# Optimization experiments

Measured on AMD Instinct MI355X. Metric: run time of the kernel, lower is better.

## Reference

```python
import jax, jax.numpy as jnp
import numpy as np

NUM_HEADS = 1
HIDDEN = 256
HEAD_DIM = HIDDEN // NUM_HEADS
SCALE = HEAD_DIM ** -0.5


def _rotate_pairwise(x):
    # (... , d) -> rotate adjacent pairs: (x0,x1,x2,x3,..) -> (-x1,x0,-x3,x2,..)
    shape = x.shape
    x = x.reshape(*shape[:-1], -1, 2)
    x = jnp.stack([-x[..., 1], x[..., 0]], axis=-1)
    return x.reshape(shape)


def setup_inputs() -> dict:
    key = jax.random.key(0)
    ks = jax.random.split(key, 12)
    B, PB, QS, KS = 1, 1, 4096, 16448
    KV_IN = 64
    d = {
        'query': jax.random.normal(ks[0], (B, PB, QS, HIDDEN), jnp.float32),
        'key': jax.random.normal(ks[1], (B, PB, KS, KV_IN), jnp.float32),
        'value': jax.random.normal(ks[2], (B, PB, KS, KV_IN), jnp.float32),
        'rope_cos': jax.random.normal(ks[3], (QS, HEAD_DIM), jnp.float32),
        'rope_sin': jax.random.normal(ks[4], (QS, HEAD_DIM), jnp.float32),
        'wq': jax.random.normal(ks[5], (HIDDEN, HIDDEN), jnp.float32) * (HIDDEN ** -0.5),
        'bq': jnp.zeros((HIDDEN,), jnp.float32),
        'wk': jax.random.normal(ks[6], (KV_IN, HIDDEN), jnp.float32) * (KV_IN ** -0.5),
        'bk': jnp.zeros((HIDDEN,), jnp.float32),
        'wv': jax.random.normal(ks[7], (KV_IN, HIDDEN), jnp.float32) * (KV_IN ** -0.5),
        'bv': jnp.zeros((HIDDEN,), jnp.float32),
        'wo': jax.random.normal(ks[8], (HIDDEN, HIDDEN), jnp.float32) * (HIDDEN ** -0.5),
        'bo': jnp.zeros((HIDDEN,), jnp.float32),
        'num_k_exclude_rope': 64,
    }
    return d


def reference(query, key, value, rope_cos, rope_sin, wq, bq, wk, bk, wv, bv, wo, bo, num_k_exclude_rope):
    batch, pb, qs, _ = query.shape
    ks = key.shape[2]
    B = batch * pb
    # projections -> [B, H, S, hd]
    q = (query @ wq + bq).reshape(B, qs, NUM_HEADS, HEAD_DIM).transpose(0, 2, 1, 3)
    k = (key @ wk + bk).reshape(B, ks, NUM_HEADS, HEAD_DIM).transpose(0, 2, 1, 3)
    v = (value @ wv + bv).reshape(B, ks, NUM_HEADS, HEAD_DIM).transpose(0, 2, 1, 3)
    cos = rope_cos[None, None]  # [1,1,QS,hd]
    sin = rope_sin[None, None]
    # split off non-RoPE keys (object pointer tokens)
    n_rot = ks - num_k_exclude_rope
    k_rot, k_pass = k[:, :, :n_rot, :], k[:, :, n_rot:, :]
    q = q * cos + _rotate_pairwise(q) * sin
    if n_rot != qs:  # rope_k_repeat branch (static shapes)
        rep = n_rot // qs
        cos_k = jnp.repeat(cos, rep, axis=2)
        sin_k = jnp.repeat(sin, rep, axis=2)
    else:
        cos_k, sin_k = cos, sin
    k_emb = k_rot * cos_k + _rotate_pairwise(k_rot) * sin_k
    k = jnp.concatenate([k_emb, k_pass], axis=-2)
    attn = jax.nn.softmax(jnp.einsum('bhqd,bhkd->bhqk', q * SCALE, k), axis=-1)
    x = jnp.einsum('bhqk,bhkd->bhqd', attn, v)
    x = x.transpose(0, 2, 1, 3).reshape(batch, pb, qs, HIDDEN)
    return x @ wo + bo
```

## Files before the change

### kernel.cpp

```cpp
#include <hip/hip_runtime.h>
#include <hip/hip_bf16.h>

typedef __attribute__((ext_vector_type(4))) float floatx4;
typedef __attribute__((ext_vector_type(8))) short shortx8;
typedef __attribute__((ext_vector_type(8))) _Float16 halfx8;
typedef _Float16 half_t;

#define MFMA_BF16(A,B,C) __builtin_amdgcn_mfma_f32_16x16x32_bf16((A),(B),(C),0,0,0)
#define NEG_INF (-__builtin_inff())
#define GLOBAL_AS __attribute__((address_space(1)))
#define LDS_AS __attribute__((address_space(3)))

static __device__ __forceinline__ unsigned short f2b(float f) {
    union { float f; unsigned u; } v; v.f = f;
    unsigned r = v.u + 0x7FFFu + ((v.u >> 16) & 1u);
    return (unsigned short)(r >> 16);
}
static __device__ __forceinline__ unsigned pack_bf16(float lo, float hi) {
    return (unsigned)f2b(lo) | ((unsigned)f2b(hi) << 16);
}
static __device__ __forceinline__ unsigned pack_half(float lo, float hi) {
    union { half_t h[2]; unsigned u; } p;
    p.h[0] = (half_t)lo; p.h[1] = (half_t)hi;
    return p.u;
}
static __device__ __forceinline__ float EXP2F(float x) { return __builtin_amdgcn_exp2f(x); }

#define NSPLIT 8
#define NSPLIT_C 16
#define NTILES 257

__global__ __launch_bounds__(256) void wtrans_kernel(
    const float* __restrict__ wq, const float* __restrict__ wk,
    const float* __restrict__ wv, const float* __restrict__ wo,
    unsigned short* __restrict__ wqt, unsigned short* __restrict__ wkt,
    unsigned short* __restrict__ wvt, unsigned short* __restrict__ wot)
{
    int gid = blockIdx.x * 256 + threadIdx.x;
    if (gid < 65536) {
        int n = gid >> 8, k = gid & 255;
        wqt[gid] = f2b(wq[k * 256 + n]);
    } else if (gid < 81920) {
        int j = gid - 65536, n = j >> 6, k = j & 63;
        wkt[j] = f2b(wk[k * 256 + n]);
    } else if (gid < 98304) {
        int j = gid - 81920, n = j >> 6, k = j & 63;
        wvt[j] = f2b(wv[k * 256 + n]);
    } else {
        int j = gid - 98304, n = j >> 8, k = j & 255;
        wot[j] = f2b(wo[k * 256 + n]);
    }
}

__global__ __launch_bounds__(256) void proj_kernel(
    const float* __restrict__ query, const float* __restrict__ key,
    const float* __restrict__ value,
    const unsigned short* __restrict__ wqt, const float* __restrict__ bq,
    const unsigned short* __restrict__ wkt, const float* __restrict__ bk,
    const unsigned short* __restrict__ wvt, const float* __restrict__ bv,
    const float* __restrict__ cosb, const float* __restrict__ sinb,
    const int* __restrict__ nkx,
    unsigned short* __restrict__ qr, unsigned short* __restrict__ krw,
    unsigned short* __restrict__ vtg)
{
    __shared__ unsigned short tbuf[256 * 72];
    const int tid = threadIdx.x;
    const int wave = tid >> 6, lane = tid & 63;
    const int c = lane & 15, quad = lane >> 4;
    const int bx = blockIdx.x;

    if (bx < 256) {
        const int m0 = (bx >> 2) * 64;
        const int n0 = (bx & 3) * 64;
        shortx8 aA[8];
        {
            const int mrow = m0 + wave * 16 + c;
            #pragma unroll
            for (int ks = 0; ks < 8; ks++) {
                const float* p = query + mrow * 256 + ks * 32 + quad * 8;
                floatx4 f0 = *(const floatx4*)p;
                floatx4 f1 = *(const floatx4*)(p + 4);
                shortx8 a;
                #pragma unroll
                for (int j = 0; j < 4; j++) { a[j] = (short)f2b(f0[j]); a[j + 4] = (short)f2b(f1[j]); }
                aA[ks] = a;
            }
        }
        floatx4 acc[4];
        #pragma unroll
        for (int nt = 0; nt < 4; nt++) { acc[nt][0]=0.f; acc[nt][1]=0.f; acc[nt][2]=0.f; acc[nt][3]=0.f; }
        #pragma unroll
        for (int nt = 0; nt < 4; nt++) {
            #pragma unroll
            for (int ks = 0; ks < 8; ks++) {
                shortx8 b = *(const shortx8*)(wqt + (n0 + nt * 16 + c) * 256 + ks * 32 + quad * 8);
                acc[nt] = MFMA_BF16(aA[ks], b, acc[nt]);
            }
        }
        const float sc = 0.09016844005556021f;
        #pragma unroll
        for (int nt = 0; nt < 4; nt++) {
            const int col = n0 + nt * 16 + c;
            float vals[4];
            #pragma unroll
            for (int r = 0; r < 4; r++) {
                const int row = m0 + wave * 16 + quad * 4 + r;
                float v = acc[nt][r] + bq[col];
                float partner = __shfl_xor(v, 1);
                float cv = cosb[row * 256 + col];
                float sn = sinb[row * 256 + col];
                float rot = (col & 1) ? partner : -partner;
                vals[r] = (v * cv + rot * sn) * sc;
            }
            #pragma unroll
            for (int r2 = 0; r2 < 4; r2 += 2) {
                float a = vals[r2], b = vals[r2 + 1];
                float ax = __shfl_xor(a, 1), bx2 = __shfl_xor(b, 1);
                float lo = (c & 1) ? bx2 : a;
                float hi = (c & 1) ? b : ax;
                int row = m0 + wave * 16 + quad * 4 + r2 + (c & 1);
                *(unsigned*)(qr + row * 256 + n0 + nt * 16 + (c & ~1)) = pack_bf16(lo, hi);
            }
        }
        return;
    }

    const int isv = (bx >= 513);
    const int m0 = (isv ? (bx - 513) : (bx - 256)) * 64;
    const float* src = isv ? value : key;
    const unsigned short* wt = isv ? wvt : wkt;
    const float* bias = isv ? bv : bk;

    shortx8 aA[2];
    {
        const int mrow = m0 + wave * 16 + c;
        #pragma unroll
        for (int ks = 0; ks < 2; ks++) {
            const float* p = src + mrow * 64 + ks * 32 + quad * 8;
            floatx4 f0 = *(const floatx4*)p;
            floatx4 f1 = *(const floatx4*)(p + 4);
            shortx8 a;
            #pragma unroll
            for (int j = 0; j < 4; j++) { a[j] = (short)f2b(f0[j]); a[j + 4] = (short)f2b(f1[j]); }
            aA[ks] = a;
        }
    }
    floatx4 acc[16];
    #pragma unroll
    for (int nt = 0; nt < 16; nt++) { acc[nt][0]=0.f; acc[nt][1]=0.f; acc[nt][2]=0.f; acc[nt][3]=0.f; }
    #pragma unroll
    for (int nt = 0; nt < 16; nt++) {
        #pragma unroll
        for (int ks = 0; ks < 2; ks++) {
            shortx8 b = *(const shortx8*)(wt + (nt * 16 + c) * 64 + ks * 32 + quad * 8);
            acc[nt] = MFMA_BF16(aA[ks], b, acc[nt]);
        }
    }
    if (!isv) {
        const int n_rot = 16448 - nkx[0];
        int rep = n_rot / 4096; if (rep < 1) rep = 1;
        int rc4[4];
        #pragma unroll
        for (int r = 0; r < 4; r++) {
            int row = m0 + wave * 16 + quad * 4 + r;
            rc4[r] = row / rep;
        }
        #pragma unroll
        for (int nt = 0; nt < 16; nt++) {
            const int col = nt * 16 + c;
            float vals[4];
            #pragma unroll
            for (int r = 0; r < 4; r++) {
                const int row = m0 + wave * 16 + quad * 4 + r;
                float v = acc[nt][r] + bias[col];
                float partner = __shfl_xor(v, 1);
                float outv = v;
                if (row < n_rot) {
                    float cv = cosb[rc4[r] * 256 + col];
                    float sn = sinb[rc4[r] * 256 + col];
                    float rot = (col & 1) ? partner : -partner;
                    outv = v * cv + rot * sn;
                }
                vals[r] = outv;
            }
            #pragma unroll
            for (int r2 = 0; r2 < 4; r2 += 2) {
                float a = vals[r2], b = vals[r2 + 1];
                float ax = __shfl_xor(a, 1), bx2 = __shfl_xor(b, 1);
                float lo = (c & 1) ? bx2 : a;
                float hi = (c & 1) ? b : ax;
                int row = m0 + wave * 16 + quad * 4 + r2 + (c & 1);
                *(unsigned*)(krw + row * 256 + nt * 16 + (c & ~1)) = pack_bf16(lo, hi);
            }
        }
    } else {
        #pragma unroll
        for (int nt = 0; nt < 16; nt++) {
            const int col = nt * 16 + c;
            #pragma unroll
            for (int r = 0; r < 4; r++) {
                const int rl = wave * 16 + quad * 4 + r;
                tbuf[col * 72 + rl] = f2b(acc[nt][r] + bias[col]);
            }
        }
        __syncthreads();
        #pragma unroll
        for (int i = 0; i < 8; i++) {
            int G = i * 256 + tid;
            int n = G >> 3, g = G & 7;
            *(floatx4*)(vtg + n * 16448 + m0 + g * 8) = *(const floatx4*)(tbuf + n * 72 + g * 8);
        }
    }
}

__global__ __launch_bounds__(512, 2) void flash_kernel(
    const unsigned short* __restrict__ qr, const unsigned short* __restrict__ kr,
    const unsigned short* __restrict__ vt, half_t* __restrict__ Opart,
    float* __restrict__ Lpart)
{
    __shared__ unsigned short smem[75776];
    const int tid = threadIdx.x;
    const int wave = tid >> 6, lane = tid & 63;
    const int c = lane & 15, quad = lane >> 4;
    const int cx = c & 7;
    const int qg = wave & 3, kvh = wave >> 2;
    const int qrow0 = blockIdx.x * 128 + qg * 32;
    const int s = blockIdx.y;
    const int t0 = (s * NTILES) / NSPLIT, t1 = ((s + 1) * NTILES) / NSPLIT;
    unsigned short* pw = smem + 65536 + wave * 1280;

    shortx8 aQ[2][8];
    #pragma unroll
    for (int u = 0; u < 2; u++)
        #pragma unroll
        for (int ks = 0; ks < 8; ks++)
            aQ[u][ks] = *(const shortx8*)(qr + (qrow0 + u * 16 + c) * 256 + ks * 32 + quad * 8);

    floatx4 o[2][16];
    #pragma unroll
    for (int u = 0; u < 2; u++)
        #pragma unroll
        for (int nt = 0; nt < 16; nt++) { o[u][nt][0]=0.f; o[u][nt][1]=0.f; o[u][nt][2]=0.f; o[u][nt][3]=0.f; }
    float l_i[2] = { 0.f, 0.f };

    auto stage = [&](int t, int buf) {
        const int kv0 = t * 64;
        unsigned short* kb = smem + buf * 16384;
        unsigned short* vb = smem + 32768 + buf * 16384;
        #pragma unroll
        for (int i = 0; i < 4; i++) {
            int L = i * 512 + tid;
            int kv = L >> 5, p = L & 31;
            int g = (p & 24) | ((p & 7) ^ (kv & 7));
            __builtin_amdgcn_global_load_lds(
                (const GLOBAL_AS void*)(const void*)(kr + (kv0 + kv) * 256 + g * 8),
                (LDS_AS void*)(void*)(kb + (i * 512 + wave * 64) * 8), 16, 0, 0);
        }
        #pragma unroll
        for (int i = 0; i < 4; i++) {
            int L = i * 512 + tid;
            int d = L >> 3, p = L & 7;
            int g = p ^ (d & 7);
            __builtin_amdgcn_global_load_lds(
                (const GLOBAL_AS void*)(const void*)(vt + d * 16448 + kv0 + g * 8),
                (LDS_AS void*)(void*)(vb + (i * 512 + wave * 64) * 8), 16, 0, 0);
        }
    };

    stage(t0, 0);
    int cur = 0;
    const int pv_p = (kvh * 4 + quad) ^ cx;
    for (int t = t0; t < t1; t++) {
        __syncthreads();
        if (t + 1 < t1) stage(t + 1, cur ^ 1);
        const unsigned short* kb = smem + cur * 16384;
        const unsigned short* vb = smem + 32768 + cur * 16384;

        floatx4 sv[2][2];
        #pragma unroll
        for (int u = 0; u < 2; u++)
            #pragma unroll
            for (int nt = 0; nt < 2; nt++) { sv[u][nt][0]=0.f; sv[u][nt][1]=0.f; sv[u][nt][2]=0.f; sv[u][nt][3]=0.f; }
        #pragma unroll
        for (int nt = 0; nt < 2; nt++) {
            const unsigned short* krow = kb + (kvh * 32 + nt * 16 + c) * 256;
            #pragma unroll
            for (int ks = 0; ks < 8; ks++) {
                int p = ((ks >> 1) * 8) | ((((ks & 1) << 2) + quad) ^ cx);
                shortx8 kfrag = *(const shortx8*)(krow + p * 8);
                sv[0][nt] = MFMA_BF16(kfrag, aQ[0][ks], sv[0][nt]);
                sv[1][nt] = MFMA_BF16(kfrag, aQ[1][ks], sv[1][nt]);
            }
        }
        #pragma unroll
        for (int u = 0; u < 2; u++) {
            float rs = 0.f;
            #pragma unroll
            for (int nt = 0; nt < 2; nt++)
                #pragma unroll
                for (int r = 0; r < 4; r++) {
                    float pv = EXP2F(sv[u][nt][r]);
                    sv[u][nt][r] = pv;
                    rs += pv;
                }
            l_i[u] += rs;
        }
        #pragma unroll
        for (int u = 0; u < 2; u++)
            #pragma unroll
            for (int nt = 0; nt < 2; nt++)
                #pragma unroll
                for (int r2 = 0; r2 < 4; r2 += 2)
                    *(unsigned*)(pw + (u * 16 + c) * 40 + nt * 16 + quad * 4 + r2) =
                        pack_bf16(sv[u][nt][r2], sv[u][nt][r2 + 1]);
        shortx8 aP[2];
        #pragma unroll
        for (int u = 0; u < 2; u++)
            aP[u] = *(const shortx8*)(pw + (u * 16 + c) * 40 + quad * 8);
        #pragma unroll
        for (int nt = 0; nt < 16; nt++) {
            const unsigned short* vrow = vb + (nt * 16 + c) * 64;
            shortx8 b0 = *(const shortx8*)(vrow + pv_p * 8);
            o[0][nt] = MFMA_BF16(aP[0], b0, o[0][nt]);
            o[1][nt] = MFMA_BF16(aP[1], b0, o[1][nt]);
        }
        cur ^= 1;
    }
    const int sEff = s * 2 + kvh;
    half_t* Ob = Opart + (size_t)sEff * (4096 * 256);
    #pragma unroll
    for (int u = 0; u < 2; u++) {
        l_i[u] += __shfl_xor(l_i[u], 16);
        l_i[u] += __shfl_xor(l_i[u], 32);
    }
    float inv[2] = { 1.0f / l_i[0], 1.0f / l_i[1] };
    #pragma unroll
    for (int u = 0; u < 2; u++) {
        float ar[4];
        #pragma unroll
        for (int r = 0; r < 4; r++) ar[r] = __shfl(inv[u], quad * 4 + r);
        #pragma unroll
        for (int nt = 0; nt < 16; nt++) {
            o[u][nt][0] *= ar[0]; o[u][nt][1] *= ar[1];
            o[u][nt][2] *= ar[2]; o[u][nt][3] *= ar[3];
        }
    }
    #pragma unroll
    for (int u = 0; u < 2; u++)
        #pragma unroll
        for (int nt = 0; nt < 16; nt++)
            #pragma unroll
            for (int r2 = 0; r2 < 4; r2 += 2) {
                float a = o[u][nt][r2], b = o[u][nt][r2 + 1];
                float ax = __shfl_xor(a, 1), bx2 = __shfl_xor(b, 1);
                float lo = (c & 1) ? bx2 : a;
                float hi = (c & 1) ? b : ax;
                int row = qrow0 + u * 16 + quad * 4 + r2 + (c & 1);
                *(unsigned*)(Ob + row * 256 + nt * 16 + (c & ~1)) = pack_half(lo, hi);
            }
    if (quad == 0) {
        #pragma unroll
        for (int u = 0; u < 2; u++)
            Lpart[sEff * 4096 + qrow0 + u * 16 + c] = l_i[u];
    }
}

__global__ __launch_bounds__(256) void finish_kernel(
    const half_t* __restrict__ Opart, const float* __restrict__ Lpart,
    const unsigned short* __restrict__ wot, const float* __restrict__ bo,
    float* __restrict__ outp)
{
    __shared__ unsigned short xb[64 * 264];
    const int tid = threadIdx.x;
    const int wave = tid >> 6, lane = tid & 63;
    const int c = lane & 15, quad = lane >> 4;
    const int m0 = blockIdx.x * 64;

    {
        const int r_l = tid >> 2;
        const int d0 = (tid & 3) * 64;
        const int row = m0 + r_l;
        float wn[NSPLIT_C], den = 0.f;
        #pragma unroll
        for (int sp = 0; sp < NSPLIT_C; sp++) { wn[sp] = Lpart[sp * 4096 + row]; den += wn[sp]; }
        float inv = 1.0f / den;
        #pragma unroll
        for (int sp = 0; sp < NSPLIT_C; sp++) wn[sp] *= inv;
        #pragma unroll
        for (int jc = 0; jc < 8; jc++) {
            float acc[8];
            #pragma unroll
            for (int j = 0; j < 8; j++) acc[j] = 0.f;
            #pragma unroll
            for (int sp = 0; sp < NSPLIT_C; sp++) {
                halfx8 hv = *(const halfx8*)(Opart + (size_t)sp * (4096 * 256) + row * 256 + d0 + jc * 8);
                #pragma unroll
                for (int j = 0; j < 8; j++) acc[j] += wn[sp] * (float)hv[j];
            }
            shortx8 xv;
            #pragma unroll
            for (int j = 0; j < 8; j++) xv[j] = (short)f2b(acc[j]);
            *(shortx8*)(xb + r_l * 264 + d0 + jc * 8) = xv;
        }
    }
    __syncthreads();
    shortx8 aX[8];
    #pragma unroll
    for (int ks = 0; ks < 8; ks++)
        aX[ks] = *(const shortx8*)(xb + (wave * 16 + c) * 264 + ks * 32 + quad * 8);
    floatx4 acc[16];
    #pragma unroll
    for (int nt = 0; nt < 16; nt++) { acc[nt][0]=0.f; acc[nt][1]=0.f; acc[nt][2]=0.f; acc[nt][3]=0.f; }
    #pragma unroll
    for (int nt = 0; nt < 16; nt++) {
        #pragma unroll
        for (int ks = 0; ks < 8; ks++) {
            shortx8 b = *(const shortx8*)(wot + (nt * 16 + c) * 256 + ks * 32 + quad * 8);
            acc[nt] = MFMA_BF16(aX[ks], b, acc[nt]);
        }
    }
    #pragma unroll
    for (int nt = 0; nt < 16; nt++) {
        const int col = nt * 16 + c;
        #pragma unroll
        for (int r = 0; r < 4; r++) {
            const int row = m0 + wave * 16 + quad * 4 + r;
            outp[row * 256 + col] = acc[nt][r] + bo[col];
        }
    }
}

extern "C" void kernel_launch(void* const* d_in, const int* in_sizes, int n_in,
                              void* d_out, int out_size, void* d_ws, size_t ws_size,
                              hipStream_t stream) {
    const float* query = (const float*)d_in[0];
    const float* key   = (const float*)d_in[1];
    const float* value = (const float*)d_in[2];
    const float* cosb  = (const float*)d_in[3];
    const float* sinb  = (const float*)d_in[4];
    const float* wq    = (const float*)d_in[5];
    const float* bq    = (const float*)d_in[6];
    const float* wk    = (const float*)d_in[7];
    const float* bk    = (const float*)d_in[8];
    const float* wv    = (const float*)d_in[9];
    const float* bv    = (const float*)d_in[10];
    const float* wo    = (const float*)d_in[11];
    const float* bo    = (const float*)d_in[12];
    const int*   nk    = (const int*)d_in[13];

    char* ws = (char*)d_ws;
    unsigned short* wqt = (unsigned short*)(ws + 0);
    unsigned short* wkt = (unsigned short*)(ws + 131072);
    unsigned short* wvt = (unsigned short*)(ws + 163840);
    unsigned short* wot = (unsigned short*)(ws + 196608);
    unsigned short* qr  = (unsigned short*)(ws + 327680);
    unsigned short* krw = (unsigned short*)(ws + 2424832);
    unsigned short* vtg = (unsigned short*)(ws + 10846208);
    half_t* Opart = (half_t*)(ws + 19267584);
    float* Lpart = (float*)(ws + 52822016);
    float* outp  = (float*)d_out;

    wtrans_kernel<<<dim3(640), dim3(256), 0, stream>>>(wq, wk, wv, wo, wqt, wkt, wvt, wot);
    proj_kernel<<<dim3(770), dim3(256), 0, stream>>>(
        query, key, value, wqt, bq, wkt, bk, wvt, bv, cosb, sinb, nk, qr, krw, vtg);
    flash_kernel<<<dim3(32, NSPLIT), dim3(512), 0, stream>>>(qr, krw, vtg, Opart, Lpart);
    finish_kernel<<<dim3(64), dim3(256), 0, stream>>>(Opart, Lpart, wot, bo, outp);
}
```

Baseline: 238.8 us.

## Split finish into parallel combine and output-projection kernels, retile weight transpose

The weight transpose now goes through an LDS tile, so global reads and writes are coalesced instead of strided. The Q projection uses 64 blocks that each cover the full 256-column width, where it previously used 256 narrower blocks. The old 64-block finish kernel is split into a 512-block combine kernel and a 64x4-block output-projection kernel, giving far more parallelism on the reduction over the 16 splits. In exchange this adds one extra launch and a bf16 intermediate round trip through the workspace, which reuses the qr buffer.

Result: faster. 230.7 us (-3.4%).

```diff
diff --git a/kernel.cpp b/kernel.cpp
--- a/kernel.cpp
+++ b/kernel.cpp
@@ -36,19 +36,38 @@
     unsigned short* __restrict__ wqt, unsigned short* __restrict__ wkt,
     unsigned short* __restrict__ wvt, unsigned short* __restrict__ wot)
 {
-    int gid = blockIdx.x * 256 + threadIdx.x;
-    if (gid < 65536) {
-        int n = gid >> 8, k = gid & 255;
-        wqt[gid] = f2b(wq[k * 256 + n]);
-    } else if (gid < 81920) {
-        int j = gid - 65536, n = j >> 6, k = j & 63;
-        wkt[j] = f2b(wk[k * 256 + n]);
-    } else if (gid < 98304) {
-        int j = gid - 81920, n = j >> 6, k = j & 63;
-        wvt[j] = f2b(wv[k * 256 + n]);
-    } else {
-        int j = gid - 98304, n = j >> 8, k = j & 255;
-        wot[j] = f2b(wo[k * 256 + n]);
+    __shared__ unsigned short tb[64 * 68];
+    const int bid = blockIdx.x, tid = threadIdx.x;
+    const float* src; unsigned short* dst; int K0, N0, Kfull;
+    if (bid < 16)      { src = wq; dst = wqt; Kfull = 256; K0 = (bid >> 2) * 64; N0 = (bid & 3) * 64; }
+    else if (bid < 20) { src = wk; dst = wkt; Kfull = 64;  K0 = 0; N0 = (bid - 16) * 64; }
+    else if (bid < 24) { src = wv; dst = wvt; Kfull = 64;  K0 = 0; N0 = (bid - 20) * 64; }
+    else { int t2 = bid - 24; src = wo; dst = wot; Kfull = 256; K0 = (t2 >> 2) * 64; N0 = (t2 & 3) * 64; }
+
+    {
+        const int r = tid >> 2, c0 = (tid & 3) * 16;
+        const float* p = src + (K0 + r) * 256 + N0 + c0;
+        #pragma unroll
+        for (int j = 0; j < 16; j += 4) {
+            floatx4 f = *(const floatx4*)(p + j);
+            tb[r * 68 + c0 + j + 0] = f2b(f[0]);
+            tb[r * 68 + c0 + j + 1] = f2b(f[1]);
+            tb[r * 68 + c0 + j + 2] = f2b(f[2]);
+            tb[r * 68 + c0 + j + 3] = f2b(f[3]);
+        }
+    }
+    __syncthreads();
+    {
+        const int n = tid >> 2, k0 = (tid & 3) * 16;
+        shortx8 v0, v1;
+        #pragma unroll
+        for (int j = 0; j < 8; j++) {
+            v0[j] = tb[(k0 + j) * 68 + n];
+            v1[j] = tb[(k0 + 8 + j) * 68 + n];
+        }
+        unsigned short* q = dst + (N0 + n) * Kfull + K0 + k0;
+        *(shortx8*)q = v0;
+        *(shortx8*)(q + 8) = v1;
     }
 }
 
@@ -69,9 +88,8 @@
     const int c = lane & 15, quad = lane >> 4;
     const int bx = blockIdx.x;
 
-    if (bx < 256) {
-        const int m0 = (bx >> 2) * 64;
-        const int n0 = (bx & 3) * 64;
+    if (bx < 64) {
+        const int m0 = bx * 64;
         shortx8 aA[8];
         {
             const int mrow = m0 + wave * 16 + c;
@@ -86,21 +104,21 @@
                 aA[ks] = a;
             }
         }
-        floatx4 acc[4];
-        #pragma unroll
-        for (int nt = 0; nt < 4; nt++) { acc[nt][0]=0.f; acc[nt][1]=0.f; acc[nt][2]=0.f; acc[nt][3]=0.f; }
-        #pragma unroll
-        for (int nt = 0; nt < 4; nt++) {
+        floatx4 acc[16];
+        #pragma unroll
+        for (int nt = 0; nt < 16; nt++) { acc[nt][0]=0.f; acc[nt][1]=0.f; acc[nt][2]=0.f; acc[nt][3]=0.f; }
+        #pragma unroll
+        for (int nt = 0; nt < 16; nt++) {
             #pragma unroll
             for (int ks = 0; ks < 8; ks++) {
-                shortx8 b = *(const shortx8*)(wqt + (n0 + nt * 16 + c) * 256 + ks * 32 + quad * 8);
+                shortx8 b = *(const shortx8*)(wqt + (nt * 16 + c) * 256 + ks * 32 + quad * 8);
                 acc[nt] = MFMA_BF16(aA[ks], b, acc[nt]);
             }
         }
         const float sc = 0.09016844005556021f;
         #pragma unroll
-        for (int nt = 0; nt < 4; nt++) {
-            const int col = n0 + nt * 16 + c;
+        for (int nt = 0; nt < 16; nt++) {
+            const int col = nt * 16 + c;
             float vals[4];
             #pragma unroll
             for (int r = 0; r < 4; r++) {
@@ -119,14 +137,14 @@
                 float lo = (c & 1) ? bx2 : a;
                 float hi = (c & 1) ? b : ax;
                 int row = m0 + wave * 16 + quad * 4 + r2 + (c & 1);
-                *(unsigned*)(qr + row * 256 + n0 + nt * 16 + (c & ~1)) = pack_bf16(lo, hi);
+                *(unsigned*)(qr + row * 256 + nt * 16 + (c & ~1)) = pack_bf16(lo, hi);
             }
         }
         return;
     }
 
-    const int isv = (bx >= 513);
-    const int m0 = (isv ? (bx - 513) : (bx - 256)) * 64;
+    const int isv = (bx >= 321);
+    const int m0 = (isv ? (bx - 321) : (bx - 64)) * 64;
     const float* src = isv ? value : key;
     const unsigned short* wt = isv ? wvt : wkt;
     const float* bias = isv ? bv : bk;
@@ -365,63 +383,62 @@
     }
 }
 
-__global__ __launch_bounds__(256) void finish_kernel(
+__global__ __launch_bounds__(256) void combine_kernel(
     const half_t* __restrict__ Opart, const float* __restrict__ Lpart,
-    const unsigned short* __restrict__ wot, const float* __restrict__ bo,
-    float* __restrict__ outp)
+    unsigned short* __restrict__ xb)
 {
-    __shared__ unsigned short xb[64 * 264];
+    int idx = blockIdx.x * 256 + threadIdx.x;
+    int row = idx >> 5;
+    int d0 = (idx & 31) * 8;
+    float wn[NSPLIT_C], den = 0.f;
+    #pragma unroll
+    for (int sp = 0; sp < NSPLIT_C; sp++) { wn[sp] = Lpart[sp * 4096 + row]; den += wn[sp]; }
+    float inv = 1.0f / den;
+    #pragma unroll
+    for (int sp = 0; sp < NSPLIT_C; sp++) wn[sp] *= inv;
+    float acc[8];
+    #pragma unroll
+    for (int j = 0; j < 8; j++) acc[j] = 0.f;
+    #pragma unroll
+    for (int sp = 0; sp < NSPLIT_C; sp++) {
+        halfx8 hv = *(const halfx8*)(Opart + (size_t)sp * (4096 * 256) + row * 256 + d0);
+        #pragma unroll
+        for (int j = 0; j < 8; j++) acc[j] += wn[sp] * (float)hv[j];
+    }
+    shortx8 xv;
+    #pragma unroll
+    for (int j = 0; j < 8; j++) xv[j] = (short)f2b(acc[j]);
+    *(shortx8*)(xb + row * 256 + d0) = xv;
+}
+
+__global__ __launch_bounds__(256) void oproj_kernel(
+    const unsigned short* __restrict__ xb, const unsigned short* __restrict__ wot,
+    const float* __restrict__ bo, float* __restrict__ outp)
+{
     const int tid = threadIdx.x;
     const int wave = tid >> 6, lane = tid & 63;
     const int c = lane & 15, quad = lane >> 4;
     const int m0 = blockIdx.x * 64;
-
-    {
-        const int r_l = tid >> 2;
-        const int d0 = (tid & 3) * 64;
-        const int row = m0 + r_l;
-        float wn[NSPLIT_C], den = 0.f;
-        #pragma unroll
-        for (int sp = 0; sp < NSPLIT_C; sp++) { wn[sp] = Lpart[sp * 4096 + row]; den += wn[sp]; }
-        float inv = 1.0f / den;
-        #pragma unroll
-        for (int sp = 0; sp < NSPLIT_C; sp++) wn[sp] *= inv;
-        #pragma unroll
-        for (int jc = 0; jc < 8; jc++) {
-            float acc[8];
-            #pragma unroll
-            for (int j = 0; j < 8; j++) acc[j] = 0.f;
-            #pragma unroll
-            for (int sp = 0; sp < NSPLIT_C; sp++) {
-                halfx8 hv = *(const halfx8*)(Opart + (size_t)sp * (4096 * 256) + row * 256 + d0 + jc * 8);
-                #pragma unroll
-                for (int j = 0; j < 8; j++) acc[j] += wn[sp] * (float)hv[j];
-            }
-            shortx8 xv;
-            #pragma unroll
-            for (int j = 0; j < 8; j++) xv[j] = (short)f2b(acc[j]);
-            *(shortx8*)(xb + r_l * 264 + d0 + jc * 8) = xv;
-        }
-    }
-    __syncthreads();
+    const int n0 = blockIdx.y * 64;
+
     shortx8 aX[8];
     #pragma unroll
     for (int ks = 0; ks < 8; ks++)
-        aX[ks] = *(const shortx8*)(xb + (wave * 16 + c) * 264 + ks * 32 + quad * 8);
-    floatx4 acc[16];
-    #pragma unroll
-    for (int nt = 0; nt < 16; nt++) { acc[nt][0]=0.f; acc[nt][1]=0.f; acc[nt][2]=0.f; acc[nt][3]=0.f; }
-    #pragma unroll
-    for (int nt = 0; nt < 16; nt++) {
+        aX[ks] = *(const shortx8*)(xb + (m0 + wave * 16 + c) * 256 + ks * 32 + quad * 8);
+    floatx4 acc[4];
+    #pragma unroll
+    for (int nt = 0; nt < 4; nt++) { acc[nt][0]=0.f; acc[nt][1]=0.f; acc[nt][2]=0.f; acc[nt][3]=0.f; }
+    #pragma unroll
+    for (int nt = 0; nt < 4; nt++) {
         #pragma unroll
         for (int ks = 0; ks < 8; ks++) {
-            shortx8 b = *(const shortx8*)(wot + (nt * 16 + c) * 256 + ks * 32 + quad * 8);
+            shortx8 b = *(const shortx8*)(wot + (n0 + nt * 16 + c) * 256 + ks * 32 + quad * 8);
             acc[nt] = MFMA_BF16(aX[ks], b, acc[nt]);
         }
     }
     #pragma unroll
-    for (int nt = 0; nt < 16; nt++) {
-        const int col = nt * 16 + c;
+    for (int nt = 0; nt < 4; nt++) {
+        const int col = n0 + nt * 16 + c;
         #pragma unroll
         for (int r = 0; r < 4; r++) {
             const int row = m0 + wave * 16 + quad * 4 + r;
@@ -454,15 +471,17 @@
     unsigned short* wvt = (unsigned short*)(ws + 163840);
     unsigned short* wot = (unsigned short*)(ws + 196608);
     unsigned short* qr  = (unsigned short*)(ws + 327680);
+    unsigned short* xb  = (unsigned short*)(ws + 327680);
     unsigned short* krw = (unsigned short*)(ws + 2424832);
     unsigned short* vtg = (unsigned short*)(ws + 10846208);
     half_t* Opart = (half_t*)(ws + 19267584);
     float* Lpart = (float*)(ws + 52822016);
     float* outp  = (float*)d_out;
 
-    wtrans_kernel<<<dim3(640), dim3(256), 0, stream>>>(wq, wk, wv, wo, wqt, wkt, wvt, wot);
-    proj_kernel<<<dim3(770), dim3(256), 0, stream>>>(
+    wtrans_kernel<<<dim3(40), dim3(256), 0, stream>>>(wq, wk, wv, wo, wqt, wkt, wvt, wot);
+    proj_kernel<<<dim3(578), dim3(256), 0, stream>>>(
         query, key, value, wqt, bq, wkt, bk, wvt, bv, cosb, sinb, nk, qr, krw, vtg);
     flash_kernel<<<dim3(32, NSPLIT), dim3(512), 0, stream>>>(qr, krw, vtg, Opart, Lpart);
-    finish_kernel<<<dim3(64), dim3(256), 0, stream>>>(Opart, Lpart, wot, bo, outp);
-}
+    combine_kernel<<<dim3(512), dim3(256), 0, stream>>>(Opart, Lpart, xb);
+    oproj_kernel<<<dim3(64, 4), dim3(256), 0, stream>>>(xb, wot, bo, outp);
+}
```
